# Optimization experiments

Measured on AMD Instinct MI355X. Metric: run time of the kernel, lower is better.

The kernel has to match this reference:

```python
import jax, jax.numpy as jnp
import numpy as np

B, N, C = 1, 32768, 256
NH, F, AG, P = 8, 32, 64, 4  # heads, cube side, agent tokens, pool size (P**3==AG)
HD = C // NH


def setup_inputs() -> dict:
    key = jax.random.key(0)
    ks = jax.random.split(key, 4)
    s = 0.02
    return {
        "x": jax.random.normal(ks[0], (B, N, C), jnp.float32),
        "w_qkv": jax.random.normal(ks[1], (3 * C, C), jnp.float32) * s,
        "b_qkv": jnp.zeros((3 * C,), jnp.float32),
        "w_proj": jax.random.normal(ks[2], (C, C), jnp.float32) * s,
        "b_proj": jnp.zeros((C,), jnp.float32),
        "w_dwc": jax.random.normal(ks[3], (C, C, 3, 3, 3), jnp.float32) * s,
        "b_dwc": jnp.zeros((C,), jnp.float32),
    }


def reference(x, w_qkv, b_qkv, w_proj, b_proj, w_dwc, b_dwc):
    scale = HD ** -0.5
    # qkv projection -> (3, B*NH, N, HD), replicating torch reshape/permute exactly
    qkv = x @ w_qkv.T + b_qkv                       # (B, N, 3C)
    qkv = qkv.reshape(B, N, 3, NH, HD)
    qkv = jnp.transpose(qkv, (2, 0, 3, 1, 4)).reshape(3, B * NH, N, HD)
    q, k, v = qkv[0], qkv[1], qkv[2]

    # agent tokens: pool q (note torch's raw reshape interleaves heads into channels)
    q_vol = q.reshape(B, F, F, F, C)                # faithful to torch reshape
    q_vol = jnp.transpose(q_vol, (0, 4, 1, 2, 3))   # (B, C, F, F, F)
    blk = F // P
    A = q_vol.reshape(B, C, P, blk, P, blk, P, blk).mean(axis=(3, 5, 7))  # (B,C,P,P,P)
    A = A.reshape(B, C, AG).transpose(0, 2, 1)      # (B, AG, C)
    A = A.reshape(B, AG, NH, HD).transpose(0, 2, 1, 3).reshape(B * NH, AG, HD)

    # stage 1: agents attend to keys, aggregate values
    agent_attn = jax.nn.softmax((A * scale) @ jnp.swapaxes(k, -2, -1), axis=-1)  # (B*NH, AG, N)
    agent_v = agent_attn @ v                        # (B*NH, AG, HD)
    # stage 2: queries attend to agents
    q_attn = jax.nn.softmax((q * scale) @ jnp.swapaxes(A, -2, -1), axis=-1)      # (B*NH, N, AG)
    o = q_attn @ agent_v                            # (B*NH, N, HD)

    # faithful to torch: transpose(1,2) then raw reshape
    o = jnp.swapaxes(o, 1, 2).reshape(B, N, C)

    # conv residual on v: (B*NH, N, HD) -> (B, C, F, F, F)
    v5 = jnp.swapaxes(v, 1, 2).reshape(B, C, F, F, F)
    conv = jax.lax.conv_general_dilated(
        v5, w_dwc, window_strides=(1, 1, 1), padding="SAME",
        dimension_numbers=("NCDHW", "OIDHW", "NCDHW"))
    conv = conv + b_dwc[None, :, None, None, None]
    o = o + jnp.transpose(conv, (0, 2, 3, 4, 1)).reshape(B, N, C)

    return o @ w_proj.T + b_proj
```

## Files before the change

### kernel.cpp

```cpp
#include <hip/hip_runtime.h>
#include <stdint.h>

typedef unsigned short u16;
typedef __attribute__((ext_vector_type(8))) short bf16x8;
typedef __attribute__((ext_vector_type(4))) float f32x4;

__device__ __forceinline__ u16 f2b(float f) {
  unsigned u = __float_as_uint(f);
  unsigned r = (u + 0x7fffu + ((u >> 16) & 1u)) >> 16;
  return (u16)r;
}
__device__ __forceinline__ float b2f(u16 s) { return __uint_as_float(((unsigned)s) << 16); }

__device__ __forceinline__ void async16(const void* g, void* l) {
  __builtin_amdgcn_global_load_lds((const __attribute__((address_space(1))) unsigned int*)g,
                                   (__attribute__((address_space(3))) unsigned int*)l, 16, 0, 0);
}


__global__ void cast_bf16(const float* __restrict__ src, u16* __restrict__ dst, int n4) {
  int i = blockIdx.x * 256 + threadIdx.x;
  if (i >= n4) return;
  const float4 v = ((const float4*)src)[i];
  uint2 o;
  o.x = (unsigned)f2b(v.x) | ((unsigned)f2b(v.y) << 16);
  o.y = (unsigned)f2b(v.z) | ((unsigned)f2b(v.w) << 16);
  ((uint2*)dst)[i] = o;
}

__global__ void pack_wc(const float* __restrict__ w, u16* __restrict__ Wc) {
  int o = blockIdx.x;
  __shared__ u16 lds[6912];
  for (int t = threadIdx.x; t < 6912; t += 256) lds[t] = f2b(w[o * 6912 + t]);
  __syncthreads();
  for (int idx = threadIdx.x; idx < 6912; idx += 256) {
    int tp = idx >> 8, i = idx & 255;
    Wc[o * 6912 + idx] = lds[i * 27 + tp];
  }
}

__global__ void pool_A(const u16* __restrict__ QKV, float* __restrict__ Apre) {
  int a = blockIdx.x >> 3, s = blockIdx.x & 7;
  int t = threadIdx.x, hp = t >> 5, dp = t & 31;
  int p1 = a >> 4, p2 = (a >> 2) & 3, p3 = a & 3;
  float sum = 0.f;
  for (int ui = 0; ui < 64; ++ui) {
    int u = s * 64 + ui;
    int f1 = p1 * 8 + (u >> 6);
    int f2 = p2 * 8 + ((u >> 3) & 7);
    int f3 = p3 * 8 + (u & 7);
    int vox = f1 * 1024 + f2 * 32 + f3;
    int n  = ((vox & 4095) << 3) + hp;
    int cq = ((vox >> 12) << 5) + dp;
    sum += b2f(QKV[n * 768 + cq]);
  }
  atomicAdd(&Apre[(hp * 64 + a) * 32 + dp], sum);
}

__global__ void pool_fin(const float* __restrict__ Apre, u16* __restrict__ Abf) {
  int idx = blockIdx.x * 256 + threadIdx.x;
  Abf[idx] = f2b(Apre[idx] * (0.17677669529663687f / 512.0f));
}

__global__ void pad_v(const u16* __restrict__ QKV, u16* __restrict__ v5) {
  int idx = blockIdx.x * 256 + threadIdx.x;
  int c8 = idx & 31, vox = idx >> 5;
  int z = vox / 1156, r2 = vox - z * 1156, y = r2 / 34, x = r2 - y * 34;
  bf16x8 val = {0, 0, 0, 0, 0, 0, 0, 0};
  if (z >= 1 && z <= 32 && y >= 1 && y <= 32 && x >= 1 && x <= 32) {
    int n = (z - 1) * 1024 + (y - 1) * 32 + (x - 1);
    val = *(const bf16x8*)(QKV + n * 768 + 512 + c8 * 8);
  }
  *(bf16x8*)(v5 + vox * 256 + c8 * 8) = val;
}

__global__ void s1_norm(const float* __restrict__ avac, const float* __restrict__ rsum,
                        u16* __restrict__ avt) {
  int idx = blockIdx.x * 256 + threadIdx.x;
  int h = idx >> 11, rem = idx & 2047, a = rem >> 5, d = rem & 31;
  avt[(h * 32 + d) * 64 + a] = f2b(avac[idx] / rsum[h * 64 + a]);
}


__device__ __forceinline__ void stage64(const u16* src, int row0, int ld, int k0,
                                        short* dst, int tid) {
  int wv = tid >> 6, lane = tid & 63;
  int r15 = lane & 15, kc8 = (lane >> 4) * 8;
#pragma unroll
  for (int j = 0; j < 4; ++j) {
    int p = j & 1, g = wv * 2 + (j >> 1);
    async16(src + (row0 + g * 16 + r15) * ld + k0 + p * 32 + kc8, dst + p * 4096 + g * 512);
  }
}

__device__ __forceinline__ void mfma64(const short* As, const short* Bs, int wm, int wn,
                                       int lane, f32x4 acc[4][4]) {
  const int q = lane >> 4, c = lane & 15;
  const int fo = q * 128 + c * 8;
#pragma unroll
  for (int p = 0; p < 2; ++p) {
    bf16x8 a[4], b[4];
#pragma unroll
    for (int mt = 0; mt < 4; ++mt) a[mt] = *(const bf16x8*)&As[p * 4096 + (wm * 4 + mt) * 512 + fo];
#pragma unroll
    for (int nt = 0; nt < 4; ++nt) b[nt] = *(const bf16x8*)&Bs[p * 4096 + (wn * 4 + nt) * 512 + fo];
#pragma unroll
    for (int mt = 0; mt < 4; ++mt)
#pragma unroll
      for (int nt = 0; nt < 4; ++nt)
        acc[mt][nt] = __builtin_amdgcn_mfma_f32_16x16x32_bf16(a[mt], b[nt], acc[mt][nt], 0, 0, 0);
  }
}

__global__ __launch_bounds__(256) void gemm_qkv(const u16* __restrict__ Xb,
                                                const u16* __restrict__ Wq,
                                                const float* __restrict__ bias,
                                                u16* __restrict__ QKV) {
  const int m0 = blockIdx.x * 128, n0 = blockIdx.y * 128;
  const int tid = threadIdx.x, lane = tid & 63, wv = tid >> 6;
  const int wm = wv >> 1, wn = wv & 1, q = lane >> 4, c = lane & 15;
  __shared__ short As[8192], Bs[8192];
  f32x4 acc[4][4] = {};
  for (int kb = 0; kb < 256; kb += 64) {
    stage64(Xb, m0, 256, kb, As, tid);
    stage64(Wq, n0, 256, kb, Bs, tid);
    __syncthreads();
    mfma64(As, Bs, wm, wn, lane, acc);
    __syncthreads();
  }
#pragma unroll
  for (int nt = 0; nt < 4; ++nt) {
    int col = n0 + wn * 64 + nt * 16 + c;
    float bv = bias[col];
#pragma unroll
    for (int mt = 0; mt < 4; ++mt) {
      int row = m0 + wm * 64 + mt * 16 + q * 4;
#pragma unroll
      for (int r = 0; r < 4; ++r) QKV[(row + r) * 768 + col] = f2b(acc[mt][nt][r] + bv);
    }
  }
}

__global__ __launch_bounds__(256) void gemm_conv(const u16* __restrict__ v5,
                                                 const u16* __restrict__ Wc,
                                                 const float* __restrict__ bias,
                                                 u16* __restrict__ Xp) {
  const int bid = blockIdx.x;
  const int xcd = bid & 7, idx = bid >> 3;
  const int n0 = (idx & 1) * 128;
  const int mt_i = xcd * 32 + (idx >> 1);
  const int m0 = mt_i * 128;
  const int z0 = mt_i >> 3, y0 = (mt_i & 7) * 4;
  const int tid = threadIdx.x, lane = tid & 63, wv = tid >> 6;
  const int wm = wv >> 1, wn = wv & 1, q = lane >> 4, c = lane & 15;
  const int r15 = lane & 15, kq8 = (lane >> 4) * 8;
  __shared__ short As[4608];
  __shared__ short Bs[12288];
  f32x4 acc[4][4] = {};
  const u16* browB = Wc + (n0 + r15) * 6912 + kq8;
  for (int dzy = 0; dzy < 9; ++dzy) {
    int dz = dzy / 3, dy = dzy - dz * 3;
    int base = (z0 + dz) * 1156 + (y0 + dy) * 34;
    int tap0 = dzy * 3;
    for (int panel = 0; panel < 8; ++panel) {
      int choff = panel * 32 + kq8;
      for (int g = wv; g < 9; g += 4) {
        int row = base + g * 16 + r15;
        row = row < 39303 ? row : 39303;
        async16(v5 + row * 256 + choff, As + g * 512);
      }
#pragma unroll
      for (int i = wv; i < 24; i += 4) {
        int dx = i >> 3, g = i & 7;
        async16(browB + g * (16 * 6912) + (tap0 + dx) * 256 + panel * 32, Bs + i * 512);
      }
      __syncthreads();
#pragma unroll
      for (int dx = 0; dx < 3; ++dx) {
        bf16x8 a[4], b[4];
#pragma unroll
        for (int mt = 0; mt < 4; ++mt) {
          int M = wm * 64 + mt * 16 + c;
          int vx = M + 2 * (M >> 5) + dx;
          a[mt] = *(const bf16x8*)&As[(vx >> 4) * 512 + q * 128 + (vx & 15) * 8];
        }
#pragma unroll
        for (int nt = 0; nt < 4; ++nt)
          b[nt] = *(const bf16x8*)&Bs[dx * 4096 + (wn * 4 + nt) * 512 + q * 128 + c * 8];
#pragma unroll
        for (int mt = 0; mt < 4; ++mt)
#pragma unroll
          for (int nt = 0; nt < 4; ++nt)
            acc[mt][nt] = __builtin_amdgcn_mfma_f32_16x16x32_bf16(a[mt], b[nt], acc[mt][nt], 0, 0, 0);
      }
      __syncthreads();
    }
  }
#pragma unroll
  for (int nt = 0; nt < 4; ++nt) {
    int col = n0 + wn * 64 + nt * 16 + c;
    float bv = bias[col];
#pragma unroll
    for (int mt = 0; mt < 4; ++mt) {
      int row = m0 + wm * 64 + mt * 16 + q * 4;
#pragma unroll
      for (int r = 0; r < 4; ++r) Xp[(row + r) * 256 + col] = f2b(acc[mt][nt][r] + bv);
    }
  }
}

__global__ __launch_bounds__(256) void gemm_proj(const u16* __restrict__ Xp,
                                                 const u16* __restrict__ Wp,
                                                 const float* __restrict__ bias,
                                                 float* __restrict__ out) {
  const int m0 = blockIdx.x * 128, n0 = blockIdx.y * 128;
  const int tid = threadIdx.x, lane = tid & 63, wv = tid >> 6;
  const int wm = wv >> 1, wn = wv & 1, q = lane >> 4, c = lane & 15;
  __shared__ short As[8192], Bs[8192];
  f32x4 acc[4][4] = {};
  for (int kb = 0; kb < 256; kb += 64) {
    stage64(Xp, m0, 256, kb, As, tid);
    stage64(Wp, n0, 256, kb, Bs, tid);
    __syncthreads();
    mfma64(As, Bs, wm, wn, lane, acc);
    __syncthreads();
  }
#pragma unroll
  for (int nt = 0; nt < 4; ++nt) {
    int col = n0 + wn * 64 + nt * 16 + c;
    float bv = bias[col];
#pragma unroll
    for (int mt = 0; mt < 4; ++mt) {
      int row = m0 + wm * 64 + mt * 16 + q * 4;
#pragma unroll
      for (int r = 0; r < 4; ++r) out[(row + r) * 256 + col] = acc[mt][nt][r] + bv;
    }
  }
}

__global__ __launch_bounds__(256) void s1_attn(const u16* __restrict__ QKV,
                                               const u16* __restrict__ Abf,
                                               float* __restrict__ avac,
                                               float* __restrict__ rsum) {
  const int h = blockIdx.y, n0 = blockIdx.x * 256;
  const int tid = threadIdx.x, lane = tid & 63, wv = tid >> 6;
  const int q = lane >> 4, c = lane & 15;
  extern __shared__ char smem[];
  u16* E  = (u16*)smem;
  u16* VT = (u16*)(smem + 33792);
  float* RED = (float*)smem;

  {
    const u16* vrow = QKV + (n0 + tid) * 768 + 512 + h * 32;
#pragma unroll
    for (int d8 = 0; d8 < 4; ++d8) {
      bf16x8 v = *(const bf16x8*)(vrow + d8 * 8);
#pragma unroll
      for (int e = 0; e < 8; ++e) VT[(d8 * 8 + e) * 264 + tid] = (u16)v[e];
    }
  }
  {
    bf16x8 af[4], bf[4];
#pragma unroll
    for (int mt = 0; mt < 4; ++mt)
      af[mt] = *(const bf16x8*)(Abf + h * 2048 + (mt * 16 + c) * 32 + q * 8);
#pragma unroll
    for (int nt = 0; nt < 4; ++nt)
      bf[nt] = *(const bf16x8*)(QKV + (n0 + wv * 64 + nt * 16 + c) * 768 + 256 + h * 32 + q * 8);
#pragma unroll
    for (int mt = 0; mt < 4; ++mt)
#pragma unroll
      for (int nt = 0; nt < 4; ++nt) {
        f32x4 s = {0.f, 0.f, 0.f, 0.f};
        s = __builtin_amdgcn_mfma_f32_16x16x32_bf16(af[mt], bf[nt], s, 0, 0, 0);
#pragma unroll
        for (int r = 0; r < 4; ++r) {
          int a = mt * 16 + q * 4 + r, nl = wv * 64 + nt * 16 + c;
          E[a * 264 + nl] = f2b(__expf(s[r]));
        }
      }
  }
  __syncthreads();
  {
    int a = tid >> 2, seg = tid & 3;
    float sum = 0.f;
    for (int i = 0; i < 64; ++i) sum += b2f(E[a * 264 + seg * 64 + i]);
    sum += __shfl_xor(sum, 1);
    sum += __shfl_xor(sum, 2);
    if (seg == 0) atomicAdd(&rsum[h * 64 + a], sum);
  }
  f32x4 pv[4][2] = {};
#pragma unroll
  for (int ks = 0; ks < 2; ++ks) {
    bf16x8 ap[4], bp[2];
#pragma unroll
    for (int mt = 0; mt < 4; ++mt)
      ap[mt] = *(const bf16x8*)&E[(mt * 16 + c) * 264 + wv * 64 + ks * 32 + q * 8];
#pragma unroll
    for (int nt = 0; nt < 2; ++nt)
      bp[nt] = *(const bf16x8*)&VT[(nt * 16 + c) * 264 + wv * 64 + ks * 32 + q * 8];
#pragma unroll
    for (int mt = 0; mt < 4; ++mt)
#pragma unroll
      for (int nt = 0; nt < 2; ++nt)
        pv[mt][nt] = __builtin_amdgcn_mfma_f32_16x16x32_bf16(ap[mt], bp[nt], pv[mt][nt], 0, 0, 0);
  }
  __syncthreads();
#pragma unroll
  for (int mt = 0; mt < 4; ++mt)
#pragma unroll
    for (int nt = 0; nt < 2; ++nt)
#pragma unroll
      for (int r = 0; r < 4; ++r)
        RED[wv * 2048 + (mt * 16 + q * 4 + r) * 32 + nt * 16 + c] = pv[mt][nt][r];
  __syncthreads();
  for (int idx = tid; idx < 2048; idx += 256) {
    float t = RED[idx] + RED[2048 + idx] + RED[4096 + idx] + RED[6144 + idx];
    atomicAdd(&avac[h * 2048 + idx], t);
  }
}

__global__ __launch_bounds__(256) void s2_attn(const u16* __restrict__ QKV,
                                               const u16* __restrict__ Abf,
                                               const u16* __restrict__ avt,
                                               u16* __restrict__ Xp) {
  const int h = blockIdx.y, n0 = blockIdx.x * 256;
  const int tid = threadIdx.x, lane = tid & 63, wv = tid >> 6;
  const int q = lane >> 4, c = lane & 15;
  extern __shared__ char smem[];
  u16* P = (u16*)smem;
  float* O = (float*)smem;

  f32x4 s[4][4];
  {
    bf16x8 af[4], bf[4];
#pragma unroll
    for (int mt = 0; mt < 4; ++mt)
      af[mt] = *(const bf16x8*)(QKV + (n0 + wv * 64 + mt * 16 + c) * 768 + h * 32 + q * 8);
#pragma unroll
    for (int nt = 0; nt < 4; ++nt)
      bf[nt] = *(const bf16x8*)(Abf + h * 2048 + (nt * 16 + c) * 32 + q * 8);
#pragma unroll
    for (int mt = 0; mt < 4; ++mt)
#pragma unroll
      for (int nt = 0; nt < 4; ++nt) {
        f32x4 z = {0.f, 0.f, 0.f, 0.f};
        s[mt][nt] = __builtin_amdgcn_mfma_f32_16x16x32_bf16(af[mt], bf[nt], z, 0, 0, 0);
      }
  }
#pragma unroll
  for (int mt = 0; mt < 4; ++mt)
#pragma unroll
    for (int r = 0; r < 4; ++r) {
      float v0 = s[mt][0][r], v1 = s[mt][1][r], v2 = s[mt][2][r], v3 = s[mt][3][r];
      float mx = fmaxf(fmaxf(v0, v1), fmaxf(v2, v3));
      mx = fmaxf(mx, __shfl_xor(mx, 1));
      mx = fmaxf(mx, __shfl_xor(mx, 2));
      mx = fmaxf(mx, __shfl_xor(mx, 4));
      mx = fmaxf(mx, __shfl_xor(mx, 8));
      float e0 = __expf(v0 - mx), e1 = __expf(v1 - mx), e2 = __expf(v2 - mx), e3 = __expf(v3 - mx);
      float sm = e0 + e1 + e2 + e3;
      sm += __shfl_xor(sm, 1);
      sm += __shfl_xor(sm, 2);
      sm += __shfl_xor(sm, 4);
      sm += __shfl_xor(sm, 8);
      float inv = 1.0f / sm;
      int tok = wv * 64 + mt * 16 + q * 4 + r;
      P[tok * 72 +      c] = f2b(e0 * inv);
      P[tok * 72 + 16 + c] = f2b(e1 * inv);
      P[tok * 72 + 32 + c] = f2b(e2 * inv);
      P[tok * 72 + 48 + c] = f2b(e3 * inv);
    }
  __syncthreads();
  f32x4 o[4][2] = {};
#pragma unroll
  for (int ks = 0; ks < 2; ++ks) {
    bf16x8 ap[4], bv[2];
#pragma unroll
    for (int mt = 0; mt < 4; ++mt)
      ap[mt] = *(const bf16x8*)&P[(wv * 64 + mt * 16 + c) * 72 + ks * 32 + q * 8];
#pragma unroll
    for (int nt = 0; nt < 2; ++nt)
      bv[nt] = *(const bf16x8*)(avt + h * 2048 + (nt * 16 + c) * 64 + ks * 32 + q * 8);
#pragma unroll
    for (int mt = 0; mt < 4; ++mt)
#pragma unroll
      for (int nt = 0; nt < 2; ++nt)
        o[mt][nt] = __builtin_amdgcn_mfma_f32_16x16x32_bf16(ap[mt], bv[nt], o[mt][nt], 0, 0, 0);
  }
  __syncthreads();
#pragma unroll
  for (int mt = 0; mt < 4; ++mt)
#pragma unroll
    for (int nt = 0; nt < 2; ++nt)
#pragma unroll
      for (int r = 0; r < 4; ++r)
        O[(nt * 16 + c) * 258 + wv * 64 + mt * 16 + q * 4 + r] = o[mt][nt][r];
  __syncthreads();
  for (int d = 0; d < 32; ++d) {
    int addr = (h * 32 + d) * 32768 + n0 + tid;
    Xp[addr] = f2b(b2f(Xp[addr]) + O[d * 258 + tid]);
  }
}


extern "C" void kernel_launch(void* const* d_in, const int* in_sizes, int n_in,
                              void* d_out, int out_size, void* d_ws, size_t ws_size,
                              hipStream_t stream) {
  const float* x      = (const float*)d_in[0];
  const float* w_qkv  = (const float*)d_in[1];
  const float* b_qkv  = (const float*)d_in[2];
  const float* w_proj = (const float*)d_in[3];
  const float* b_proj = (const float*)d_in[4];
  const float* w_dwc  = (const float*)d_in[5];
  const float* b_dwc  = (const float*)d_in[6];
  float* out = (float*)d_out;
  char* ws = (char*)d_ws;

  u16* Xb   = (u16*)(ws);
  u16* QKV  = (u16*)(ws + 16777216);
  u16* V5   = (u16*)(ws + 67108864);
  u16* Wc   = (u16*)(ws + 87232512);
  u16* Wqb  = (u16*)(ws + 90771456);
  u16* Wpb  = (u16*)(ws + 91164672);
  u16* Abf  = (u16*)(ws + 91295744);
  u16* AVT  = (u16*)(ws + 91328512);
  float* AVAC = (float*)(ws + 91361280);
  float* RSUM = (float*)(ws + 91426816);
  float* APRE = (float*)(ws + 91428864);
  u16* Xp = Xb;

  hipMemsetAsync(AVAC, 0, 65536 + 2048 + 65536, stream);
  cast_bf16<<<8192, 256, 0, stream>>>(x, Xb, 2097152);
  cast_bf16<<<192, 256, 0, stream>>>(w_qkv, Wqb, 49152);
  cast_bf16<<<64, 256, 0, stream>>>(w_proj, Wpb, 16384);
  pack_wc<<<256, 256, 0, stream>>>(w_dwc, Wc);
  gemm_qkv<<<dim3(256, 6), 256, 0, stream>>>(Xb, Wqb, b_qkv, QKV);
  pool_A<<<512, 256, 0, stream>>>(QKV, APRE);
  pool_fin<<<64, 256, 0, stream>>>(APRE, Abf);
  pad_v<<<4913, 256, 0, stream>>>(QKV, V5);
  s1_attn<<<dim3(128, 8), 256, 50688, stream>>>(QKV, Abf, AVAC, RSUM);
  s1_norm<<<64, 256, 0, stream>>>(AVAC, RSUM, AVT);
  gemm_conv<<<512, 256, 0, stream>>>(V5, Wc, b_dwc, Xp);
  s2_attn<<<dim3(128, 8), 256, 36864, stream>>>(QKV, Abf, AVT, Xp);
  gemm_proj<<<dim3(256, 2), 256, 0, stream>>>(Xp, Wpb, b_proj, out);
}
```

Before: 348.6 us.

## Split conv GEMM over K into two partial outputs, fold pool finalize and weight casts

New measurement: 365.1 us. 1.05x slower.

```diff
diff --git a/kernel.cpp b/kernel.cpp
--- a/kernel.cpp
+++ b/kernel.cpp
@@ -4,6 +4,8 @@
 typedef unsigned short u16;
 typedef __attribute__((ext_vector_type(8))) short bf16x8;
 typedef __attribute__((ext_vector_type(4))) float f32x4;
+
+#define KSCALE (0.17677669529663687f / 512.0f)
 
 __device__ __forceinline__ u16 f2b(float f) {
   unsigned u = __float_as_uint(f);
@@ -17,10 +19,31 @@
                                    (__attribute__((address_space(3))) unsigned int*)l, 16, 0, 0);
 }
 
+__device__ __forceinline__ bf16x8 frag8(const float* p, float k) {
+  float4 f0 = *(const float4*)p, f1 = *(const float4*)(p + 4);
+  bf16x8 v;
+  v[0] = f2b(f0.x * k); v[1] = f2b(f0.y * k); v[2] = f2b(f0.z * k); v[3] = f2b(f0.w * k);
+  v[4] = f2b(f1.x * k); v[5] = f2b(f1.y * k); v[6] = f2b(f1.z * k); v[7] = f2b(f1.w * k);
+  return v;
+}
+
 
 __global__ void cast_bf16(const float* __restrict__ src, u16* __restrict__ dst, int n4) {
   int i = blockIdx.x * 256 + threadIdx.x;
   if (i >= n4) return;
+  const float4 v = ((const float4*)src)[i];
+  uint2 o;
+  o.x = (unsigned)f2b(v.x) | ((unsigned)f2b(v.y) << 16);
+  o.y = (unsigned)f2b(v.z) | ((unsigned)f2b(v.w) << 16);
+  ((uint2*)dst)[i] = o;
+}
+
+__global__ void cast_w(const float* __restrict__ wq, const float* __restrict__ wp,
+                       u16* __restrict__ dq, u16* __restrict__ dp) {
+  int b = blockIdx.x;
+  const float* src = b < 192 ? wq : wp;
+  u16* dst = b < 192 ? dq : dp;
+  int i = (b < 192 ? b : b - 192) * 256 + threadIdx.x;
   const float4 v = ((const float4*)src)[i];
   uint2 o;
   o.x = (unsigned)f2b(v.x) | ((unsigned)f2b(v.y) << 16);
@@ -55,11 +78,6 @@
     sum += b2f(QKV[n * 768 + cq]);
   }
   atomicAdd(&Apre[(hp * 64 + a) * 32 + dp], sum);
-}
-
-__global__ void pool_fin(const float* __restrict__ Apre, u16* __restrict__ Abf) {
-  int idx = blockIdx.x * 256 + threadIdx.x;
-  Abf[idx] = f2b(Apre[idx] * (0.17677669529663687f / 512.0f));
 }
 
 __global__ void pad_v(const u16* __restrict__ QKV, u16* __restrict__ v5) {
@@ -143,12 +161,13 @@
 
 __global__ __launch_bounds__(256) void gemm_conv(const u16* __restrict__ v5,
                                                  const u16* __restrict__ Wc,
-                                                 const float* __restrict__ bias,
-                                                 u16* __restrict__ Xp) {
+                                                 u16* __restrict__ P0,
+                                                 u16* __restrict__ P1) {
   const int bid = blockIdx.x;
-  const int xcd = bid & 7, idx = bid >> 3;
-  const int n0 = (idx & 1) * 128;
-  const int mt_i = xcd * 32 + (idx >> 1);
+  const int xcd = bid & 7, rest = bid >> 3;
+  const int kk = rest & 1;
+  const int n0 = ((rest >> 1) & 1) * 128;
+  const int mt_i = xcd * 32 + (rest >> 2);
   const int m0 = mt_i * 128;
   const int z0 = mt_i >> 3, y0 = (mt_i & 7) * 4;
   const int tid = threadIdx.x, lane = tid & 63, wv = tid >> 6;
@@ -162,7 +181,8 @@
     int dz = dzy / 3, dy = dzy - dz * 3;
     int base = (z0 + dz) * 1156 + (y0 + dy) * 34;
     int tap0 = dzy * 3;
-    for (int panel = 0; panel < 8; ++panel) {
+    for (int pp = 0; pp < 4; ++pp) {
+      int panel = kk * 4 + pp;
       int choff = panel * 32 + kq8;
       for (int g = wv; g < 9; g += 4) {
         int row = base + g * 16 + r15;
@@ -196,15 +216,15 @@
       __syncthreads();
     }
   }
+  u16* P = kk ? P1 : P0;
 #pragma unroll
   for (int nt = 0; nt < 4; ++nt) {
     int col = n0 + wn * 64 + nt * 16 + c;
-    float bv = bias[col];
 #pragma unroll
     for (int mt = 0; mt < 4; ++mt) {
       int row = m0 + wm * 64 + mt * 16 + q * 4;
 #pragma unroll
-      for (int r = 0; r < 4; ++r) Xp[(row + r) * 256 + col] = f2b(acc[mt][nt][r] + bv);
+      for (int r = 0; r < 4; ++r) P[(row + r) * 256 + col] = f2b(acc[mt][nt][r]);
     }
   }
 }
@@ -239,7 +259,7 @@
 }
 
 __global__ __launch_bounds__(256) void s1_attn(const u16* __restrict__ QKV,
-                                               const u16* __restrict__ Abf,
+                                               const float* __restrict__ Apre,
                                                float* __restrict__ avac,
                                                float* __restrict__ rsum) {
   const int h = blockIdx.y, n0 = blockIdx.x * 256;
@@ -263,7 +283,7 @@
     bf16x8 af[4], bf[4];
 #pragma unroll
     for (int mt = 0; mt < 4; ++mt)
-      af[mt] = *(const bf16x8*)(Abf + h * 2048 + (mt * 16 + c) * 32 + q * 8);
+      af[mt] = frag8(Apre + h * 2048 + (mt * 16 + c) * 32 + q * 8, KSCALE);
 #pragma unroll
     for (int nt = 0; nt < 4; ++nt)
       bf[nt] = *(const bf16x8*)(QKV + (n0 + wv * 64 + nt * 16 + c) * 768 + 256 + h * 32 + q * 8);
@@ -321,8 +341,11 @@
 }
 
 __global__ __launch_bounds__(256) void s2_attn(const u16* __restrict__ QKV,
-                                               const u16* __restrict__ Abf,
+                                               const float* __restrict__ Apre,
                                                const u16* __restrict__ avt,
+                                               const u16* __restrict__ P0,
+                                               const u16* __restrict__ P1,
+                                               const float* __restrict__ bdwc,
                                                u16* __restrict__ Xp) {
   const int h = blockIdx.y, n0 = blockIdx.x * 256;
   const int tid = threadIdx.x, lane = tid & 63, wv = tid >> 6;
@@ -339,7 +362,7 @@
       af[mt] = *(const bf16x8*)(QKV + (n0 + wv * 64 + mt * 16 + c) * 768 + h * 32 + q * 8);
 #pragma unroll
     for (int nt = 0; nt < 4; ++nt)
-      bf[nt] = *(const bf16x8*)(Abf + h * 2048 + (nt * 16 + c) * 32 + q * 8);
+      bf[nt] = frag8(Apre + h * 2048 + (nt * 16 + c) * 32 + q * 8, KSCALE);
 #pragma unroll
     for (int mt = 0; mt < 4; ++mt)
 #pragma unroll
@@ -397,9 +420,11 @@
       for (int r = 0; r < 4; ++r)
         O[(nt * 16 + c) * 258 + wv * 64 + mt * 16 + q * 4 + r] = o[mt][nt][r];
   __syncthreads();
+  float bias = bdwc[tid];
   for (int d = 0; d < 32; ++d) {
     int addr = (h * 32 + d) * 32768 + n0 + tid;
-    Xp[addr] = f2b(b2f(Xp[addr]) + O[d * 258 + tid]);
+    float base = b2f(P0[addr]) + b2f(P1[addr]) + bias;
+    Xp[addr] = f2b(base + O[d * 258 + tid]);
   }
 }
 
@@ -423,25 +448,24 @@
   u16* Wc   = (u16*)(ws + 87232512);
   u16* Wqb  = (u16*)(ws + 90771456);
   u16* Wpb  = (u16*)(ws + 91164672);
-  u16* Abf  = (u16*)(ws + 91295744);
   u16* AVT  = (u16*)(ws + 91328512);
   float* AVAC = (float*)(ws + 91361280);
   float* RSUM = (float*)(ws + 91426816);
   float* APRE = (float*)(ws + 91428864);
+  u16* P1   = (u16*)(ws + 91500544);
+  u16* P0 = Xb;
   u16* Xp = Xb;
 
   hipMemsetAsync(AVAC, 0, 65536 + 2048 + 65536, stream);
   cast_bf16<<<8192, 256, 0, stream>>>(x, Xb, 2097152);
-  cast_bf16<<<192, 256, 0, stream>>>(w_qkv, Wqb, 49152);
-  cast_bf16<<<64, 256, 0, stream>>>(w_proj, Wpb, 16384);
+  cast_w<<<256, 256, 0, stream>>>(w_qkv, w_proj, Wqb, Wpb);
   pack_wc<<<256, 256, 0, stream>>>(w_dwc, Wc);
   gemm_qkv<<<dim3(256, 6), 256, 0, stream>>>(Xb, Wqb, b_qkv, QKV);
   pool_A<<<512, 256, 0, stream>>>(QKV, APRE);
-  pool_fin<<<64, 256, 0, stream>>>(APRE, Abf);
   pad_v<<<4913, 256, 0, stream>>>(QKV, V5);
-  s1_attn<<<dim3(128, 8), 256, 50688, stream>>>(QKV, Abf, AVAC, RSUM);
+  s1_attn<<<dim3(128, 8), 256, 50688, stream>>>(QKV, APRE, AVAC, RSUM);
   s1_norm<<<64, 256, 0, stream>>>(AVAC, RSUM, AVT);
-  gemm_conv<<<512, 256, 0, stream>>>(V5, Wc, b_dwc, Xp);
-  s2_attn<<<dim3(128, 8), 256, 36864, stream>>>(QKV, Abf, AVT, Xp);
+  gemm_conv<<<1024, 256, 0, stream>>>(V5, Wc, P0, P1);
+  s2_attn<<<dim3(128, 8), 256, 36864, stream>>>(QKV, APRE, AVT, P0, P1, b_dwc, Xp);
   gemm_proj<<<dim3(256, 2), 256, 0, stream>>>(Xp, Wpb, b_proj, out);
 }
```

## Merge small kernels and co-schedule conv with stage-1 attention in one launch

Applied to the files above, without the earlier changes.

Result: no change. 346.5 us (-0.6%).

```diff
diff --git a/kernel.cpp b/kernel.cpp
--- a/kernel.cpp
+++ b/kernel.cpp
@@ -4,6 +4,8 @@
 typedef unsigned short u16;
 typedef __attribute__((ext_vector_type(8))) short bf16x8;
 typedef __attribute__((ext_vector_type(4))) float f32x4;
+
+#define KSCALE (0.17677669529663687f / 512.0f)
 
 __device__ __forceinline__ u16 f2b(float f) {
   unsigned u = __float_as_uint(f);
@@ -17,68 +19,72 @@
                                    (__attribute__((address_space(3))) unsigned int*)l, 16, 0, 0);
 }
 
-
-__global__ void cast_bf16(const float* __restrict__ src, u16* __restrict__ dst, int n4) {
-  int i = blockIdx.x * 256 + threadIdx.x;
-  if (i >= n4) return;
-  const float4 v = ((const float4*)src)[i];
-  uint2 o;
-  o.x = (unsigned)f2b(v.x) | ((unsigned)f2b(v.y) << 16);
-  o.y = (unsigned)f2b(v.z) | ((unsigned)f2b(v.w) << 16);
-  ((uint2*)dst)[i] = o;
-}
-
-__global__ void pack_wc(const float* __restrict__ w, u16* __restrict__ Wc) {
-  int o = blockIdx.x;
-  __shared__ u16 lds[6912];
-  for (int t = threadIdx.x; t < 6912; t += 256) lds[t] = f2b(w[o * 6912 + t]);
-  __syncthreads();
-  for (int idx = threadIdx.x; idx < 6912; idx += 256) {
-    int tp = idx >> 8, i = idx & 255;
-    Wc[o * 6912 + idx] = lds[i * 27 + tp];
-  }
-}
-
-__global__ void pool_A(const u16* __restrict__ QKV, float* __restrict__ Apre) {
-  int a = blockIdx.x >> 3, s = blockIdx.x & 7;
-  int t = threadIdx.x, hp = t >> 5, dp = t & 31;
-  int p1 = a >> 4, p2 = (a >> 2) & 3, p3 = a & 3;
-  float sum = 0.f;
-  for (int ui = 0; ui < 64; ++ui) {
-    int u = s * 64 + ui;
-    int f1 = p1 * 8 + (u >> 6);
-    int f2 = p2 * 8 + ((u >> 3) & 7);
-    int f3 = p3 * 8 + (u & 7);
-    int vox = f1 * 1024 + f2 * 32 + f3;
-    int n  = ((vox & 4095) << 3) + hp;
-    int cq = ((vox >> 12) << 5) + dp;
-    sum += b2f(QKV[n * 768 + cq]);
-  }
-  atomicAdd(&Apre[(hp * 64 + a) * 32 + dp], sum);
-}
-
-__global__ void pool_fin(const float* __restrict__ Apre, u16* __restrict__ Abf) {
-  int idx = blockIdx.x * 256 + threadIdx.x;
-  Abf[idx] = f2b(Apre[idx] * (0.17677669529663687f / 512.0f));
-}
-
-__global__ void pad_v(const u16* __restrict__ QKV, u16* __restrict__ v5) {
-  int idx = blockIdx.x * 256 + threadIdx.x;
-  int c8 = idx & 31, vox = idx >> 5;
-  int z = vox / 1156, r2 = vox - z * 1156, y = r2 / 34, x = r2 - y * 34;
-  bf16x8 val = {0, 0, 0, 0, 0, 0, 0, 0};
-  if (z >= 1 && z <= 32 && y >= 1 && y <= 32 && x >= 1 && x <= 32) {
-    int n = (z - 1) * 1024 + (y - 1) * 32 + (x - 1);
-    val = *(const bf16x8*)(QKV + n * 768 + 512 + c8 * 8);
-  }
-  *(bf16x8*)(v5 + vox * 256 + c8 * 8) = val;
-}
-
-__global__ void s1_norm(const float* __restrict__ avac, const float* __restrict__ rsum,
-                        u16* __restrict__ avt) {
-  int idx = blockIdx.x * 256 + threadIdx.x;
-  int h = idx >> 11, rem = idx & 2047, a = rem >> 5, d = rem & 31;
-  avt[(h * 32 + d) * 64 + a] = f2b(avac[idx] / rsum[h * 64 + a]);
+__device__ __forceinline__ bf16x8 frag8(const float* p, float k) {
+  float4 f0 = *(const float4*)p, f1 = *(const float4*)(p + 4);
+  bf16x8 v;
+  v[0] = f2b(f0.x * k); v[1] = f2b(f0.y * k); v[2] = f2b(f0.z * k); v[3] = f2b(f0.w * k);
+  v[4] = f2b(f1.x * k); v[5] = f2b(f1.y * k); v[6] = f2b(f1.z * k); v[7] = f2b(f1.w * k);
+  return v;
+}
+
+__global__ void prep_cast(const float* __restrict__ x, const float* __restrict__ wq,
+                          const float* __restrict__ wp, const float* __restrict__ wdwc,
+                          u16* __restrict__ Xb, u16* __restrict__ Wqb,
+                          u16* __restrict__ Wpb, u16* __restrict__ Wc) {
+  int b = blockIdx.x, tid = threadIdx.x;
+  if (b < 8448) {
+    const float* src; u16* dst; int i;
+    if (b < 8192)      { src = x;  dst = Xb;  i = b * 256 + tid; }
+    else if (b < 8384) { src = wq; dst = Wqb; i = (b - 8192) * 256 + tid; }
+    else               { src = wp; dst = Wpb; i = (b - 8384) * 256 + tid; }
+    const float4 v = ((const float4*)src)[i];
+    uint2 o;
+    o.x = (unsigned)f2b(v.x) | ((unsigned)f2b(v.y) << 16);
+    o.y = (unsigned)f2b(v.z) | ((unsigned)f2b(v.w) << 16);
+    ((uint2*)dst)[i] = o;
+  } else {
+    int o = b - 8448;
+    __shared__ u16 lds[6912];
+    for (int t = tid; t < 6912; t += 256) lds[t] = f2b(wdwc[o * 6912 + t]);
+    __syncthreads();
+    for (int idx = tid; idx < 6912; idx += 256) {
+      int tp = idx >> 8, i = idx & 255;
+      Wc[o * 6912 + idx] = lds[i * 27 + tp];
+    }
+  }
+}
+
+__global__ void prep_av(const u16* __restrict__ QKV, u16* __restrict__ v5,
+                        float* __restrict__ Apre) {
+  int b = blockIdx.x, tid = threadIdx.x;
+  if (b < 4913) {
+    int idx = b * 256 + tid;
+    int c8 = idx & 31, vox = idx >> 5;
+    int z = vox / 1156, r2 = vox - z * 1156, y = r2 / 34, x = r2 - y * 34;
+    bf16x8 val = {0, 0, 0, 0, 0, 0, 0, 0};
+    if (z >= 1 && z <= 32 && y >= 1 && y <= 32 && x >= 1 && x <= 32) {
+      int n = (z - 1) * 1024 + (y - 1) * 32 + (x - 1);
+      val = *(const bf16x8*)(QKV + n * 768 + 512 + c8 * 8);
+    }
+    *(bf16x8*)(v5 + vox * 256 + c8 * 8) = val;
+  } else {
+    int b2 = b - 4913;
+    int a = b2 >> 3, s = b2 & 7;
+    int hp = tid >> 5, dp = tid & 31;
+    int p1 = a >> 4, p2 = (a >> 2) & 3, p3 = a & 3;
+    float sum = 0.f;
+    for (int ui = 0; ui < 64; ++ui) {
+      int u = s * 64 + ui;
+      int f1 = p1 * 8 + (u >> 6);
+      int f2 = p2 * 8 + ((u >> 3) & 7);
+      int f3 = p3 * 8 + (u & 7);
+      int vox = f1 * 1024 + f2 * 32 + f3;
+      int n  = ((vox & 4095) << 3) + hp;
+      int cq = ((vox >> 12) << 5) + dp;
+      sum += b2f(QKV[n * 768 + cq]);
+    }
+    atomicAdd(&Apre[(hp * 64 + a) * 32 + dp], sum);
+  }
 }
 
 
@@ -141,70 +147,152 @@
   }
 }
 
-__global__ __launch_bounds__(256) void gemm_conv(const u16* __restrict__ v5,
-                                                 const u16* __restrict__ Wc,
-                                                 const float* __restrict__ bias,
-                                                 u16* __restrict__ Xp) {
-  const int bid = blockIdx.x;
-  const int xcd = bid & 7, idx = bid >> 3;
-  const int n0 = (idx & 1) * 128;
-  const int mt_i = xcd * 32 + (idx >> 1);
-  const int m0 = mt_i * 128;
-  const int z0 = mt_i >> 3, y0 = (mt_i & 7) * 4;
+__global__ __launch_bounds__(256) void conv_s1(const u16* __restrict__ v5,
+                                               const u16* __restrict__ Wc,
+                                               const float* __restrict__ bias,
+                                               u16* __restrict__ Xp,
+                                               const u16* __restrict__ QKV,
+                                               const float* __restrict__ Apre,
+                                               float* __restrict__ avac,
+                                               float* __restrict__ rsum) {
+  extern __shared__ char smem[];
   const int tid = threadIdx.x, lane = tid & 63, wv = tid >> 6;
-  const int wm = wv >> 1, wn = wv & 1, q = lane >> 4, c = lane & 15;
-  const int r15 = lane & 15, kq8 = (lane >> 4) * 8;
-  __shared__ short As[4608];
-  __shared__ short Bs[12288];
-  f32x4 acc[4][4] = {};
-  const u16* browB = Wc + (n0 + r15) * 6912 + kq8;
-  for (int dzy = 0; dzy < 9; ++dzy) {
-    int dz = dzy / 3, dy = dzy - dz * 3;
-    int base = (z0 + dz) * 1156 + (y0 + dy) * 34;
-    int tap0 = dzy * 3;
-    for (int panel = 0; panel < 8; ++panel) {
-      int choff = panel * 32 + kq8;
-      for (int g = wv; g < 9; g += 4) {
-        int row = base + g * 16 + r15;
-        row = row < 39303 ? row : 39303;
-        async16(v5 + row * 256 + choff, As + g * 512);
+  const int q = lane >> 4, c = lane & 15;
+  if (blockIdx.x < 512) {
+    const int bid = blockIdx.x;
+    const int xcd = bid & 7, idx = bid >> 3;
+    const int n0 = (idx & 1) * 128;
+    const int mt_i = xcd * 32 + (idx >> 1);
+    const int m0 = mt_i * 128;
+    const int z0 = mt_i >> 3, y0 = (mt_i & 7) * 4;
+    const int wm = wv >> 1, wn = wv & 1;
+    const int r15 = lane & 15, kq8 = (lane >> 4) * 8;
+    short* As = (short*)smem;
+    short* Bs = (short*)(smem + 9216);
+    f32x4 acc[4][4] = {};
+    const u16* browB = Wc + (n0 + r15) * 6912 + kq8;
+    for (int dzy = 0; dzy < 9; ++dzy) {
+      int dz = dzy / 3, dy = dzy - dz * 3;
+      int base = (z0 + dz) * 1156 + (y0 + dy) * 34;
+      int tap0 = dzy * 3;
+      for (int panel = 0; panel < 8; ++panel) {
+        int choff = panel * 32 + kq8;
+        for (int g = wv; g < 9; g += 4) {
+          int row = base + g * 16 + r15;
+          row = row < 39303 ? row : 39303;
+          async16(v5 + row * 256 + choff, As + g * 512);
+        }
+#pragma unroll
+        for (int i = wv; i < 24; i += 4) {
+          int dx = i >> 3, g = i & 7;
+          async16(browB + g * (16 * 6912) + (tap0 + dx) * 256 + panel * 32, Bs + i * 512);
+        }
+        __syncthreads();
+#pragma unroll
+        for (int dx = 0; dx < 3; ++dx) {
+          bf16x8 a[4], b[4];
+#pragma unroll
+          for (int mt = 0; mt < 4; ++mt) {
+            int M = wm * 64 + mt * 16 + c;
+            int vx = M + 2 * (M >> 5) + dx;
+            a[mt] = *(const bf16x8*)&As[(vx >> 4) * 512 + q * 128 + (vx & 15) * 8];
+          }
+#pragma unroll
+          for (int nt = 0; nt < 4; ++nt)
+            b[nt] = *(const bf16x8*)&Bs[dx * 4096 + (wn * 4 + nt) * 512 + q * 128 + c * 8];
+#pragma unroll
+          for (int mt = 0; mt < 4; ++mt)
+#pragma unroll
+            for (int nt = 0; nt < 4; ++nt)
+              acc[mt][nt] = __builtin_amdgcn_mfma_f32_16x16x32_bf16(a[mt], b[nt], acc[mt][nt], 0, 0, 0);
+        }
+        __syncthreads();
       }
-#pragma unroll
-      for (int i = wv; i < 24; i += 4) {
-        int dx = i >> 3, g = i & 7;
-        async16(browB + g * (16 * 6912) + (tap0 + dx) * 256 + panel * 32, Bs + i * 512);
+    }
+#pragma unroll
+    for (int nt = 0; nt < 4; ++nt) {
+      int col = n0 + wn * 64 + nt * 16 + c;
+      float bv = bias[col];
+#pragma unroll
+      for (int mt = 0; mt < 4; ++mt) {
+        int row = m0 + wm * 64 + mt * 16 + q * 4;
+#pragma unroll
+        for (int r = 0; r < 4; ++r) Xp[(row + r) * 256 + col] = f2b(acc[mt][nt][r] + bv);
       }
-      __syncthreads();
-#pragma unroll
-      for (int dx = 0; dx < 3; ++dx) {
-        bf16x8 a[4], b[4];
-#pragma unroll
-        for (int mt = 0; mt < 4; ++mt) {
-          int M = wm * 64 + mt * 16 + c;
-          int vx = M + 2 * (M >> 5) + dx;
-          a[mt] = *(const bf16x8*)&As[(vx >> 4) * 512 + q * 128 + (vx & 15) * 8];
+    }
+  } else {
+    const int vb = blockIdx.x - 512;
+    const int h = vb >> 7, n0 = (vb & 127) * 256;
+    u16* E  = (u16*)smem;
+    u16* VT = (u16*)(smem + 33792);
+    float* RED = (float*)smem;
+    {
+      const u16* vrow = QKV + (n0 + tid) * 768 + 512 + h * 32;
+#pragma unroll
+      for (int d8 = 0; d8 < 4; ++d8) {
+        bf16x8 v = *(const bf16x8*)(vrow + d8 * 8);
+#pragma unroll
+        for (int e = 0; e < 8; ++e) VT[(d8 * 8 + e) * 264 + tid] = (u16)v[e];
+      }
+    }
+    {
+      bf16x8 af[4], bf[4];
+#pragma unroll
+      for (int mt = 0; mt < 4; ++mt)
+        af[mt] = frag8(Apre + h * 2048 + (mt * 16 + c) * 32 + q * 8, KSCALE);
+#pragma unroll
+      for (int nt = 0; nt < 4; ++nt)
+        bf[nt] = *(const bf16x8*)(QKV + (n0 + wv * 64 + nt * 16 + c) * 768 + 256 + h * 32 + q * 8);
+#pragma unroll
+      for (int mt = 0; mt < 4; ++mt)
+#pragma unroll
+        for (int nt = 0; nt < 4; ++nt) {
+          f32x4 s = {0.f, 0.f, 0.f, 0.f};
+          s = __builtin_amdgcn_mfma_f32_16x16x32_bf16(af[mt], bf[nt], s, 0, 0, 0);
+#pragma unroll
+          for (int r = 0; r < 4; ++r) {
+            int a = mt * 16 + q * 4 + r, nl = wv * 64 + nt * 16 + c;
+            E[a * 264 + nl] = f2b(__expf(s[r]));
+          }
         }
-#pragma unroll
-        for (int nt = 0; nt < 4; ++nt)
-          b[nt] = *(const bf16x8*)&Bs[dx * 4096 + (wn * 4 + nt) * 512 + q * 128 + c * 8];
-#pragma unroll
-        for (int mt = 0; mt < 4; ++mt)
-#pragma unroll
-          for (int nt = 0; nt < 4; ++nt)
-            acc[mt][nt] = __builtin_amdgcn_mfma_f32_16x16x32_bf16(a[mt], b[nt], acc[mt][nt], 0, 0, 0);
-      }
-      __syncthreads();
-    }
-  }
-#pragma unroll
-  for (int nt = 0; nt < 4; ++nt) {
-    int col = n0 + wn * 64 + nt * 16 + c;
-    float bv = bias[col];
-#pragma unroll
-    for (int mt = 0; mt < 4; ++mt) {
-      int row = m0 + wm * 64 + mt * 16 + q * 4;
-#pragma unroll
-      for (int r = 0; r < 4; ++r) Xp[(row + r) * 256 + col] = f2b(acc[mt][nt][r] + bv);
+    }
+    __syncthreads();
+    {
+      int a = tid >> 2, seg = tid & 3;
+      float sum = 0.f;
+      for (int i = 0; i < 64; ++i) sum += b2f(E[a * 264 + seg * 64 + i]);
+      sum += __shfl_xor(sum, 1);
+      sum += __shfl_xor(sum, 2);
+      if (seg == 0) atomicAdd(&rsum[h * 64 + a], sum);
+    }
+    f32x4 pv[4][2] = {};
+#pragma unroll
+    for (int ks = 0; ks < 2; ++ks) {
+      bf16x8 ap[4], bp[2];
+#pragma unroll
+      for (int mt = 0; mt < 4; ++mt)
+        ap[mt] = *(const bf16x8*)&E[(mt * 16 + c) * 264 + wv * 64 + ks * 32 + q * 8];
+#pragma unroll
+      for (int nt = 0; nt < 2; ++nt)
+        bp[nt] = *(const bf16x8*)&VT[(nt * 16 + c) * 264 + wv * 64 + ks * 32 + q * 8];
+#pragma unroll
+      for (int mt = 0; mt < 4; ++mt)
+#pragma unroll
+        for (int nt = 0; nt < 2; ++nt)
+          pv[mt][nt] = __builtin_amdgcn_mfma_f32_16x16x32_bf16(ap[mt], bp[nt], pv[mt][nt], 0, 0, 0);
+    }
+    __syncthreads();
+#pragma unroll
+    for (int mt = 0; mt < 4; ++mt)
+#pragma unroll
+      for (int nt = 0; nt < 2; ++nt)
+#pragma unroll
+        for (int r = 0; r < 4; ++r)
+          RED[wv * 2048 + (mt * 16 + q * 4 + r) * 32 + nt * 16 + c] = pv[mt][nt][r];
+    __syncthreads();
+    for (int idx = tid; idx < 2048; idx += 256) {
+      float t = RED[idx] + RED[2048 + idx] + RED[4096 + idx] + RED[6144 + idx];
+      atomicAdd(&avac[h * 2048 + idx], t);
     }
   }
 }
@@ -238,91 +326,10 @@
   }
 }
 
-__global__ __launch_bounds__(256) void s1_attn(const u16* __restrict__ QKV,
-                                               const u16* __restrict__ Abf,
-                                               float* __restrict__ avac,
-                                               float* __restrict__ rsum) {
-  const int h = blockIdx.y, n0 = blockIdx.x * 256;
-  const int tid = threadIdx.x, lane = tid & 63, wv = tid >> 6;
-  const int q = lane >> 4, c = lane & 15;
-  extern __shared__ char smem[];
-  u16* E  = (u16*)smem;
-  u16* VT = (u16*)(smem + 33792);
-  float* RED = (float*)smem;
-
-  {
-    const u16* vrow = QKV + (n0 + tid) * 768 + 512 + h * 32;
-#pragma unroll
-    for (int d8 = 0; d8 < 4; ++d8) {
-      bf16x8 v = *(const bf16x8*)(vrow + d8 * 8);
-#pragma unroll
-      for (int e = 0; e < 8; ++e) VT[(d8 * 8 + e) * 264 + tid] = (u16)v[e];
-    }
-  }
-  {
-    bf16x8 af[4], bf[4];
-#pragma unroll
-    for (int mt = 0; mt < 4; ++mt)
-      af[mt] = *(const bf16x8*)(Abf + h * 2048 + (mt * 16 + c) * 32 + q * 8);
-#pragma unroll
-    for (int nt = 0; nt < 4; ++nt)
-      bf[nt] = *(const bf16x8*)(QKV + (n0 + wv * 64 + nt * 16 + c) * 768 + 256 + h * 32 + q * 8);
-#pragma unroll
-    for (int mt = 0; mt < 4; ++mt)
-#pragma unroll
-      for (int nt = 0; nt < 4; ++nt) {
-        f32x4 s = {0.f, 0.f, 0.f, 0.f};
-        s = __builtin_amdgcn_mfma_f32_16x16x32_bf16(af[mt], bf[nt], s, 0, 0, 0);
-#pragma unroll
-        for (int r = 0; r < 4; ++r) {
-          int a = mt * 16 + q * 4 + r, nl = wv * 64 + nt * 16 + c;
-          E[a * 264 + nl] = f2b(__expf(s[r]));
-        }
-      }
-  }
-  __syncthreads();
-  {
-    int a = tid >> 2, seg = tid & 3;
-    float sum = 0.f;
-    for (int i = 0; i < 64; ++i) sum += b2f(E[a * 264 + seg * 64 + i]);
-    sum += __shfl_xor(sum, 1);
-    sum += __shfl_xor(sum, 2);
-    if (seg == 0) atomicAdd(&rsum[h * 64 + a], sum);
-  }
-  f32x4 pv[4][2] = {};
-#pragma unroll
-  for (int ks = 0; ks < 2; ++ks) {
-    bf16x8 ap[4], bp[2];
-#pragma unroll
-    for (int mt = 0; mt < 4; ++mt)
-      ap[mt] = *(const bf16x8*)&E[(mt * 16 + c) * 264 + wv * 64 + ks * 32 + q * 8];
-#pragma unroll
-    for (int nt = 0; nt < 2; ++nt)
-      bp[nt] = *(const bf16x8*)&VT[(nt * 16 + c) * 264 + wv * 64 + ks * 32 + q * 8];
-#pragma unroll
-    for (int mt = 0; mt < 4; ++mt)
-#pragma unroll
-      for (int nt = 0; nt < 2; ++nt)
-        pv[mt][nt] = __builtin_amdgcn_mfma_f32_16x16x32_bf16(ap[mt], bp[nt], pv[mt][nt], 0, 0, 0);
-  }
-  __syncthreads();
-#pragma unroll
-  for (int mt = 0; mt < 4; ++mt)
-#pragma unroll
-    for (int nt = 0; nt < 2; ++nt)
-#pragma unroll
-      for (int r = 0; r < 4; ++r)
-        RED[wv * 2048 + (mt * 16 + q * 4 + r) * 32 + nt * 16 + c] = pv[mt][nt][r];
-  __syncthreads();
-  for (int idx = tid; idx < 2048; idx += 256) {
-    float t = RED[idx] + RED[2048 + idx] + RED[4096 + idx] + RED[6144 + idx];
-    atomicAdd(&avac[h * 2048 + idx], t);
-  }
-}
-
 __global__ __launch_bounds__(256) void s2_attn(const u16* __restrict__ QKV,
-                                               const u16* __restrict__ Abf,
-                                               const u16* __restrict__ avt,
+                                               const float* __restrict__ Apre,
+                                               const float* __restrict__ avac,
+                                               const float* __restrict__ rsum,
                                                u16* __restrict__ Xp) {
   const int h = blockIdx.y, n0 = blockIdx.x * 256;
   const int tid = threadIdx.x, lane = tid & 63, wv = tid >> 6;
@@ -330,6 +337,13 @@
   extern __shared__ char smem[];
   u16* P = (u16*)smem;
   float* O = (float*)smem;
+  u16* AVT = (u16*)(smem + 36864);
+
+  for (int j = 0; j < 8; ++j) {
+    int i = j * 256 + tid;
+    int a = i >> 5, d = i & 31;
+    AVT[d * 72 + a] = f2b(avac[h * 2048 + i] / rsum[h * 64 + a]);
+  }
 
   f32x4 s[4][4];
   {
@@ -339,7 +353,7 @@
       af[mt] = *(const bf16x8*)(QKV + (n0 + wv * 64 + mt * 16 + c) * 768 + h * 32 + q * 8);
 #pragma unroll
     for (int nt = 0; nt < 4; ++nt)
-      bf[nt] = *(const bf16x8*)(Abf + h * 2048 + (nt * 16 + c) * 32 + q * 8);
+      bf[nt] = frag8(Apre + h * 2048 + (nt * 16 + c) * 32 + q * 8, KSCALE);
 #pragma unroll
     for (int mt = 0; mt < 4; ++mt)
 #pragma unroll
@@ -381,7 +395,7 @@
       ap[mt] = *(const bf16x8*)&P[(wv * 64 + mt * 16 + c) * 72 + ks * 32 + q * 8];
 #pragma unroll
     for (int nt = 0; nt < 2; ++nt)
-      bv[nt] = *(const bf16x8*)(avt + h * 2048 + (nt * 16 + c) * 64 + ks * 32 + q * 8);
+      bv[nt] = *(const bf16x8*)&AVT[(nt * 16 + c) * 72 + ks * 32 + q * 8];
 #pragma unroll
     for (int mt = 0; mt < 4; ++mt)
 #pragma unroll
@@ -423,25 +437,16 @@
   u16* Wc   = (u16*)(ws + 87232512);
   u16* Wqb  = (u16*)(ws + 90771456);
   u16* Wpb  = (u16*)(ws + 91164672);
-  u16* Abf  = (u16*)(ws + 91295744);
-  u16* AVT  = (u16*)(ws + 91328512);
   float* AVAC = (float*)(ws + 91361280);
   float* RSUM = (float*)(ws + 91426816);
   float* APRE = (float*)(ws + 91428864);
   u16* Xp = Xb;
 
   hipMemsetAsync(AVAC, 0, 65536 + 2048 + 65536, stream);
-  cast_bf16<<<8192, 256, 0, stream>>>(x, Xb, 2097152);
-  cast_bf16<<<192, 256, 0, stream>>>(w_qkv, Wqb, 49152);
-  cast_bf16<<<64, 256, 0, stream>>>(w_proj, Wpb, 16384);
-  pack_wc<<<256, 256, 0, stream>>>(w_dwc, Wc);
+  prep_cast<<<8704, 256, 0, stream>>>(x, w_qkv, w_proj, w_dwc, Xb, Wqb, Wpb, Wc);
   gemm_qkv<<<dim3(256, 6), 256, 0, stream>>>(Xb, Wqb, b_qkv, QKV);
-  pool_A<<<512, 256, 0, stream>>>(QKV, APRE);
-  pool_fin<<<64, 256, 0, stream>>>(APRE, Abf);
-  pad_v<<<4913, 256, 0, stream>>>(QKV, V5);
-  s1_attn<<<dim3(128, 8), 256, 50688, stream>>>(QKV, Abf, AVAC, RSUM);
-  s1_norm<<<64, 256, 0, stream>>>(AVAC, RSUM, AVT);
-  gemm_conv<<<512, 256, 0, stream>>>(V5, Wc, b_dwc, Xp);
-  s2_attn<<<dim3(128, 8), 256, 36864, stream>>>(QKV, Abf, AVT, Xp);
+  prep_av<<<5425, 256, 0, stream>>>(QKV, V5, APRE);
+  conv_s1<<<2560, 256, 50688, stream>>>(V5, Wc, b_dwc, Xp, QKV, APRE, AVAC, RSUM);
+  s2_attn<<<dim3(128, 8), 256, 41472, stream>>>(QKV, APRE, AVAC, RSUM, Xp);
   gemm_proj<<<dim3(256, 2), 256, 0, stream>>>(Xp, Wpb, b_proj, out);
 }
```
